# Kernel tuning notes

Measured on AMD Instinct MI355X. Metric: run time of the kernel, lower is better.

The kernel has to match this reference:

```python
import jax, jax.numpy as jnp
import numpy as np

# SOM hyperparameters (from init_kwargs)
M_ROWS = 64
N_COLS = 64
DIM = 256
MAX_EPOCHS = 100
INITIAL_RADIUS = 32.0  # max(m, n) / 2
INITIAL_LR = 0.1
STD_COEFF = 0.5
BATCH = 8192

# [m*n, 2] integer grid locations (constant, non-differentiable)
_LOC_VECTS = jnp.asarray(
    np.stack(np.meshgrid(np.arange(M_ROWS), np.arange(N_COLS), indexing='ij'), axis=-1).reshape(-1, 2),
    dtype=jnp.int32,
)


def setup_inputs() -> dict:
    key = jax.random.key(0)
    k1, k2 = jax.random.split(key)
    return {
        'input_vect': jax.random.normal(k1, (BATCH, DIM), dtype=jnp.float32),
        'weights': jax.random.normal(k2, (M_ROWS * N_COLS, DIM), dtype=jnp.float32),
        'epoch': 10,
    }


def reference(input_vect, weights, epoch):
    # squared_distance[b, m] = sum_d (weights[m, d] - x[b, d])^2  -> [B, M]
    sq_dist = (
        jnp.sum(input_vect * input_vect, axis=1, keepdims=True)
        - 2.0 * (input_vect @ weights.T)
        + jnp.sum(weights * weights, axis=1)[None, :]
    )
    bmu_indices = jnp.argmin(sq_dist, axis=1)             # [B]
    bmu_locs = _LOC_VECTS[bmu_indices]                    # [B, 2]

    ep = jnp.float32(epoch)
    radius = INITIAL_RADIUS - ep * ((INITIAL_RADIUS - 1.0) / (MAX_EPOCHS - 1.0))
    alpha = INITIAL_LR * (1.0 - ep / MAX_EPOCHS)

    # bmu_distance_squares[b, m] = ||locs[m] - bmu_locs[b]||^2  -> [B, M]
    diff = _LOC_VECTS[None, :, :] - bmu_locs[:, None, :]  # int [B, M, 2]
    bmu_dist_sq = jnp.sum(diff * diff, axis=2).astype(jnp.float32)

    denom_nf = 2.0 * jnp.square(radius * STD_COEFF)
    learning_rate_op = jnp.exp(-bmu_dist_sq / denom_nf) * alpha  # [B, M]

    # numerator[m, d] = sum_b lr[b, m] * x[b, d]
    numerator = jnp.einsum('bm,bd->md', learning_rate_op, input_vect)
    denominator = jnp.sum(learning_rate_op, axis=0)[:, None] + 1e-12  # [M, 1]
    new_weights = numerator / denominator
    return bmu_locs, new_weights
```

## Files before the change

kernel.cpp:

```cpp
#include <hip/hip_runtime.h>
#include <stdint.h>

#define DIM   256
#define BATCH 8192
#define MCELL 4096

typedef unsigned long long u64;
typedef unsigned short u16;
typedef __attribute__((ext_vector_type(8))) short bf16x8;
typedef __attribute__((ext_vector_type(4))) float f32x4;

__device__ __forceinline__ u64 packMin(float v, unsigned idx) {
    unsigned u = __float_as_uint(v);
    u = (u & 0x80000000u) ? ~u : (u | 0x80000000u);
    return ((u64)u << 32) | (u64)idx;
}
__device__ __forceinline__ u16 f2bf(float f) {
    unsigned u = __float_as_uint(f);
    u += 0x7fffu + ((u >> 16) & 1u);
    return (u16)(u >> 16);
}
__device__ __forceinline__ void gll16(const void* g, const char* l) {
    __builtin_amdgcn_global_load_lds(
        (const __attribute__((address_space(1))) unsigned int*)g,
        (__attribute__((address_space(3))) unsigned int*)l, 16, 0, 0);
}
__device__ __forceinline__ u64 umin64(u64 a, u64 b) { return a < b ? a : b; }
__device__ __forceinline__ u64 umax64(u64 a, u64 b) { return a < b ? b : a; }
__device__ __forceinline__ void merge3(u64& a1, u64& a2, u64& a3,
                                       u64 o1, u64 o2, u64 o3) {
    u64 L1 = umin64(a1, o1), H1 = umax64(a1, o1);
    u64 L2 = umin64(a2, o2);
    u64 L3 = umin64(a3, o3);
    a1 = L1;
    a2 = umin64(H1, L2);
    a3 = umin64(umax64(H1, L2), L3);
}

__global__ void k_prep(const float* __restrict__ X, const float* __restrict__ W,
                       u16* __restrict__ Xh, u16* __restrict__ Wh,
                       float* __restrict__ w2, const int* __restrict__ epoch_p,
                       float* __restrict__ scal) {
    const int blk = blockIdx.x;
    const int t = threadIdx.x;
    if (blk == 3072) {
        int raw = epoch_p[0];
        float ep = (raw >= 0 && raw < 100000) ? (float)raw : __int_as_float(raw);
        float radius = 32.0f - ep * (31.0f / 99.0f);
        float alpha  = 0.1f * (1.0f - ep / 100.0f);
        float rs = radius * 0.5f;
        float denom = 2.0f * rs * rs;
        if (t < 64)       scal[t]  = expf(-((float)(t * t)) / denom);
        else if (t == 64) scal[64] = alpha;
        return;
    }
    if (blk < 2048) {
        const int fi = blk * 256 + t;
        float4 v = ((const float4*)X)[fi];
        ushort4 h = {f2bf(v.x), f2bf(v.y), f2bf(v.z), f2bf(v.w)};
        ((ushort4*)Xh)[fi] = h;
    } else {
        const int fi = (blk - 2048) * 256 + t;
        float4 v = ((const float4*)W)[fi];
        ushort4 h = {f2bf(v.x), f2bf(v.y), f2bf(v.z), f2bf(v.w)};
        ((ushort4*)Wh)[fi] = h;
        float s = v.x * v.x + v.y * v.y + v.z * v.z + v.w * v.w;
        #pragma unroll
        for (int off = 32; off; off >>= 1) s += __shfl_down(s, off);
        if ((t & 63) == 0) w2[fi >> 6] = s;
    }
}

__global__ __launch_bounds__(256, 3)
void k_gemm_argmin(const u16* __restrict__ Xh, const u16* __restrict__ Wh,
                   const float* __restrict__ w2, u64* __restrict__ slots) {
    __shared__ char smem[49152];
    const int wg = blockIdx.x;
    const int swz = (wg & 7) * 256 + (wg >> 3);
    const int bt = swz >> 5;
    const int mt = swz & 31;
    const int tid = threadIdx.x;
    const int wid = tid >> 6;
    const int lane = tid & 63;
    const int wr = wid >> 1, wc = wid & 1;
    const int b0 = bt * 128, m0 = mt * 128;
    const int m0w = m0 + wc * 64;

    const int sr0 = wid * 32 + (lane >> 2);
    const int sr1 = sr0 + 16;
    const int ss  = lane & 3;
    const int sg0 = ss ^ ((sr0 >> 1) & 3);
    const int sg1 = ss ^ ((sr1 >> 1) & 3);
    const size_t gA0 = (size_t)(b0 + sr0) * DIM + sg0 * 8;
    const size_t gA1 = (size_t)(b0 + sr1) * DIM + sg1 * 8;
    const size_t gB0 = (size_t)(m0 + sr0) * DIM + sg0 * 8;
    const size_t gB1 = (size_t)(m0 + sr1) * DIM + sg1 * 8;
    const int ldsA = wid * 2048;

    const int rl = lane & 15, g = lane >> 4;
    const int slot = g ^ ((rl >> 1) & 3);
    const int aoff = (wr * 64 + rl) * 64 + slot * 16;
    const int boff = (wc * 64 + rl) * 64 + slot * 16;

    f32x4 acc[4][4];
    #pragma unroll
    for (int i = 0; i < 4; ++i)
        #pragma unroll
        for (int j = 0; j < 4; ++j) acc[i][j] = (f32x4){0.f, 0.f, 0.f, 0.f};

    #define STAGE(buf, c) do {                                                \
        char* base_ = smem + (buf) * 16384;                                   \
        const int co_ = (c) * 32;                                             \
        gll16(Xh + gA0 + co_, base_ + ldsA);                                  \
        gll16(Xh + gA1 + co_, base_ + ldsA + 1024);                           \
        gll16(Wh + gB0 + co_, base_ + 8192 + ldsA);                           \
        gll16(Wh + gB1 + co_, base_ + 8192 + ldsA + 1024);                    \
    } while (0)

    STAGE(0, 0);
    STAGE(1, 1);
    #pragma unroll
    for (int c = 0; c < 8; ++c) {
        if (c < 6) {
            STAGE((c + 2) % 3, c + 2);
            asm volatile("s_waitcnt vmcnt(8)" ::: "memory");
        } else if (c == 6) {
            asm volatile("s_waitcnt vmcnt(4)" ::: "memory");
        } else {
            asm volatile("s_waitcnt vmcnt(0)" ::: "memory");
        }
        __builtin_amdgcn_sched_barrier(0);
        __builtin_amdgcn_s_barrier();

        const char* bufc = smem + (c % 3) * 16384;
        bf16x8 ah[4];
        #pragma unroll
        for (int i = 0; i < 4; ++i)
            ah[i] = *(const bf16x8*)(bufc + aoff + i * 1024);
        __builtin_amdgcn_s_setprio(1);
        #pragma unroll
        for (int j = 0; j < 4; ++j) {
            const bf16x8 bh = *(const bf16x8*)(bufc + 8192 + boff + j * 1024);
            #pragma unroll
            for (int i = 0; i < 4; ++i)
                acc[i][j] = __builtin_amdgcn_mfma_f32_16x16x32_bf16(ah[i], bh, acc[i][j], 0, 0, 0);
        }
        __builtin_amdgcn_s_setprio(0);
        __builtin_amdgcn_s_barrier();
    }
    #undef STAGE

    float w2v[4];
    #pragma unroll
    for (int j = 0; j < 4; ++j) w2v[j] = w2[m0w + j * 16 + rl];

    __syncthreads();
    u64* ex = (u64*)smem;

    #pragma unroll
    for (int i = 0; i < 4; ++i) {
        #pragma unroll
        for (int q = 0; q < 4; ++q) {
            u64 t1 = ~0ull, t2 = ~0ull, t3 = ~0ull;
            #pragma unroll
            for (int j = 0; j < 4; ++j) {
                const float d = w2v[j] - 2.0f * acc[i][j][q];
                const u64 p = packMin(d, (unsigned)(m0w + j * 16 + rl));
                if (p < t1)      { t3 = t2; t2 = t1; t1 = p; }
                else if (p < t2) { t3 = t2; t2 = p; }
                else if (p < t3) { t3 = p; }
            }
            #pragma unroll
            for (int off = 1; off <= 8; off <<= 1) {
                const u64 o1 = __shfl_xor(t1, off);
                const u64 o2 = __shfl_xor(t2, off);
                const u64 o3 = __shfl_xor(t3, off);
                merge3(t1, t2, t3, o1, o2, o3);
            }
            if (rl == 0) {
                const int rloc = wr * 64 + i * 16 + g * 4 + q;
                u64* e = ex + (rloc * 2 + wc) * 3;
                e[0] = t1; e[1] = t2; e[2] = t3;
            }
        }
    }
    __syncthreads();
    if (tid < 128) {
        const u64* e0 = ex + (tid * 2 + 0) * 3;
        const u64* e1 = ex + (tid * 2 + 1) * 3;
        u64 a1 = e0[0], a2 = e0[1], a3 = e0[2];
        merge3(a1, a2, a3, e1[0], e1[1], e1[2]);
        const size_t row = b0 + tid;
        slots[row * 96 +      mt] = a1;
        slots[row * 96 + 32 + mt] = a2;
        slots[row * 96 + 64 + mt] = a3;
    }
}

__global__ void k_merge(const u64* __restrict__ slots, const float* __restrict__ X,
                        const float* __restrict__ W, const float* __restrict__ w2,
                        float* __restrict__ out_locs, float* __restrict__ A,
                        float* __restrict__ cnt) {
    const int wid = threadIdx.x >> 6, l = threadIdx.x & 63;
    const int row = blockIdx.x * 4 + wid;
    u64 t1, t2, t3;
    if (l < 32) {
        const u64* s = slots + (size_t)row * 96;
        t1 = s[l]; t2 = s[32 + l]; t3 = s[64 + l];
    } else { t1 = t2 = t3 = ~0ull; }
    #pragma unroll
    for (int off = 1; off <= 32; off <<= 1) {
        const u64 o1 = __shfl_xor(t1, off);
        const u64 o2 = __shfl_xor(t2, off);
        const u64 o3 = __shfl_xor(t3, off);
        merge3(t1, t2, t3, o1, o2, o3);
    }
    const int cand[3] = {(int)(t1 & 0xFFFFFFFFull), (int)(t2 & 0xFFFFFFFFull),
                         (int)(t3 & 0xFFFFFFFFull)};
    const float4 xv = *(const float4*)(X + (size_t)row * DIM + l * 4);
    float bd = 0.0f; int bm = -1;
    #pragma unroll
    for (int tix = 0; tix < 3; ++tix) {
        const int mc = cand[tix];
        const float4 wv = *(const float4*)(W + (size_t)mc * DIM + l * 4);
        float s = xv.x * wv.x + xv.y * wv.y + xv.z * wv.z + xv.w * wv.w;
        #pragma unroll
        for (int off = 1; off <= 32; off <<= 1) s += __shfl_xor(s, off);
        const float d = w2[mc] - 2.0f * s;
        if (bm < 0 || d < bd || (d == bd && mc < bm)) { bd = d; bm = mc; }
    }
    if (l == 0) {
        out_locs[row * 2 + 0] = (float)(bm >> 6);
        out_locs[row * 2 + 1] = (float)(bm & 63);
        atomicAdd(&cnt[bm], 1.0f);
    }
    float* ap = A + (size_t)bm * DIM + l * 4;
    atomicAdd(ap + 0, xv.x);
    atomicAdd(ap + 1, xv.y);
    atomicAdd(ap + 2, xv.z);
    atomicAdd(ap + 3, xv.w);
}

__global__ void k_conv1(const float* __restrict__ A, const float* __restrict__ E,
                        float* __restrict__ T1, const float* __restrict__ cnt,
                        float* __restrict__ c1) {
    if (blockIdx.x >= 4096) {
        int t = (blockIdx.x - 4096) * 256 + threadIdx.x;
        int gi = t >> 6, mj = t & 63;
        float acc = 0.0f;
        #pragma unroll
        for (int gj = 0; gj < 64; ++gj) {
            int dd = mj - gj; dd = dd < 0 ? -dd : dd;
            acc += E[dd] * cnt[gi * 64 + gj];
        }
        c1[gi * 64 + mj] = acc;
        return;
    }
    __shared__ float Es[64];
    const int d = threadIdx.x;
    if (d < 64) Es[d] = E[d];
    __syncthreads();
    const int gi = blockIdx.x >> 6, mj = blockIdx.x & 63;
    const float* base = A + (size_t)gi * 64 * DIM + d;
    float acc = 0.0f;
    #pragma unroll
    for (int gj = 0; gj < 64; ++gj) {
        int dd = mj - gj; dd = dd < 0 ? -dd : dd;
        acc += Es[dd] * base[(size_t)gj * DIM];
    }
    T1[(size_t)blockIdx.x * DIM + d] = acc;
}

__global__ void k_conv2(const float* __restrict__ T1, const float* __restrict__ scal,
                        const float* __restrict__ c1, float* __restrict__ outw) {
    __shared__ float Es[64];
    __shared__ float salpha;
    const int d = threadIdx.x;
    if (d < 64) Es[d] = scal[d];
    if (d == 64) salpha = scal[64];
    __syncthreads();
    const int mi = blockIdx.x >> 6, mj = blockIdx.x & 63;
    float acc = 0.0f, den = 0.0f;
    #pragma unroll
    for (int gi = 0; gi < 64; ++gi) {
        int dd = mi - gi; dd = dd < 0 ? -dd : dd;
        acc += Es[dd] * T1[((size_t)gi * 64 + mj) * DIM + d];
        den += Es[dd] * c1[gi * 64 + mj];
    }
    const float a = salpha;
    const float v = (a * acc) / (a * den + 1e-12f);
    outw[((size_t)mi * 64 + mj) * DIM + d] = v;
}

extern "C" void kernel_launch(void* const* d_in, const int* in_sizes, int n_in,
                              void* d_out, int out_size, void* d_ws, size_t ws_size,
                              hipStream_t stream) {
    const float* X = (const float*)d_in[0];
    const float* W = (const float*)d_in[1];
    const int*   ep = (const int*)d_in[2];
    float* out = (float*)d_out;

    char* ws = (char*)d_ws;
    u64*   slots = (u64*)(ws + 0);
    u16*   Xh   = (u16*)(ws + 6291456);
    float* A    = (float*)(ws + 6291456);
    float* cnt  = (float*)(ws + 10485760);
    u16*   Wh   = (u16*)(ws + 10502144);
    float* w2   = (float*)(ws + 12599296);
    float* scal = (float*)(ws + 12615680);
    float* c1   = (float*)(ws + 12616192);
    float* T1   = (float*)(ws + 0);

    k_prep<<<3073, 256, 0, stream>>>(X, W, Xh, Wh, w2, ep, scal);
    k_gemm_argmin<<<2048, 256, 0, stream>>>(Xh, Wh, w2, slots);
    hipMemsetAsync(ws + 6291456, 0, 4194304 + 16384, stream);
    k_merge<<<2048, 256, 0, stream>>>(slots, X, W, w2, out, A, cnt);
    k_conv1<<<4112, 256, 0, stream>>>(A, scal, T1, cnt, c1);
    k_conv2<<<4096, 256, 0, stream>>>(T1, scal, c1, out + 16384);
}
```

Measured before the change: 200.5 us.

## Transpose GEMM operand roles and keep top-2 candidates per tile instead of top-3

Swaps the MFMA operand roles so each lane's accumulators run along the codebook dimension for a fixed batch column. This lets each thread do most of the per-row argmin in registers and cuts the cross-lane shuffle reduction to two steps. Each tile now keeps the two best candidates instead of three, which shrinks the slots buffer and the merge kernel's loads. The merge kernel still refines the final candidates in exact fp32, but keeping fewer bf16 candidates raises the chance of picking a different BMU on near-ties.

```diff
diff --git a/kernel.cpp b/kernel.cpp
--- a/kernel.cpp
+++ b/kernel.cpp
@@ -27,6 +27,16 @@
 }
 __device__ __forceinline__ u64 umin64(u64 a, u64 b) { return a < b ? a : b; }
 __device__ __forceinline__ u64 umax64(u64 a, u64 b) { return a < b ? b : a; }
+__device__ __forceinline__ void ins2(u64& t1, u64& t2, u64 p) {
+    u64 hi = umax64(p, t1);
+    t1 = umin64(p, t1);
+    t2 = umin64(t2, hi);
+}
+__device__ __forceinline__ void merge2(u64& a1, u64& a2, u64 o1, u64 o2) {
+    u64 H1 = umax64(a1, o1);
+    a1 = umin64(a1, o1);
+    a2 = umin64(H1, umin64(a2, o2));
+}
 __device__ __forceinline__ void merge3(u64& a1, u64& a2, u64& a3,
                                        u64 o1, u64 o2, u64 o3) {
     u64 L1 = umin64(a1, o1), H1 = umax64(a1, o1);
@@ -84,7 +94,6 @@
     const int lane = tid & 63;
     const int wr = wid >> 1, wc = wid & 1;
     const int b0 = bt * 128, m0 = mt * 128;
-    const int m0w = m0 + wc * 64;
 
     const int sr0 = wid * 32 + (lane >> 2);
     const int sr1 = sr0 + 16;
@@ -99,8 +108,8 @@
 
     const int rl = lane & 15, g = lane >> 4;
     const int slot = g ^ ((rl >> 1) & 3);
-    const int aoff = (wr * 64 + rl) * 64 + slot * 16;
-    const int boff = (wc * 64 + rl) * 64 + slot * 16;
+    const int xoff = (wc * 64 + rl) * 64 + slot * 16;
+    const int woff = (wr * 64 + rl) * 64 + slot * 16;
 
     f32x4 acc[4][4];
     #pragma unroll
@@ -133,67 +142,59 @@
         __builtin_amdgcn_s_barrier();
 
         const char* bufc = smem + (c % 3) * 16384;
-        bf16x8 ah[4];
+        bf16x8 wf[4];
         #pragma unroll
         for (int i = 0; i < 4; ++i)
-            ah[i] = *(const bf16x8*)(bufc + aoff + i * 1024);
+            wf[i] = *(const bf16x8*)(bufc + 8192 + woff + i * 1024);
         __builtin_amdgcn_s_setprio(1);
         #pragma unroll
         for (int j = 0; j < 4; ++j) {
-            const bf16x8 bh = *(const bf16x8*)(bufc + 8192 + boff + j * 1024);
+            const bf16x8 xf = *(const bf16x8*)(bufc + xoff + j * 1024);
             #pragma unroll
             for (int i = 0; i < 4; ++i)
-                acc[i][j] = __builtin_amdgcn_mfma_f32_16x16x32_bf16(ah[i], bh, acc[i][j], 0, 0, 0);
+                acc[i][j] = __builtin_amdgcn_mfma_f32_16x16x32_bf16(wf[i], xf, acc[i][j], 0, 0, 0);
         }
         __builtin_amdgcn_s_setprio(0);
         __builtin_amdgcn_s_barrier();
     }
     #undef STAGE
 
-    float w2v[4];
-    #pragma unroll
-    for (int j = 0; j < 4; ++j) w2v[j] = w2[m0w + j * 16 + rl];
+    float w2v[16];
+    #pragma unroll
+    for (int ii = 0; ii < 16; ++ii)
+        w2v[ii] = w2[m0 + wr * 64 + (ii >> 2) * 16 + g * 4 + (ii & 3)];
 
     __syncthreads();
     u64* ex = (u64*)smem;
 
     #pragma unroll
-    for (int i = 0; i < 4; ++i) {
-        #pragma unroll
-        for (int q = 0; q < 4; ++q) {
-            u64 t1 = ~0ull, t2 = ~0ull, t3 = ~0ull;
+    for (int j = 0; j < 4; ++j) {
+        u64 t1 = ~0ull, t2 = ~0ull;
+        #pragma unroll
+        for (int i = 0; i < 4; ++i)
             #pragma unroll
-            for (int j = 0; j < 4; ++j) {
-                const float d = w2v[j] - 2.0f * acc[i][j][q];
-                const u64 p = packMin(d, (unsigned)(m0w + j * 16 + rl));
-                if (p < t1)      { t3 = t2; t2 = t1; t1 = p; }
-                else if (p < t2) { t3 = t2; t2 = p; }
-                else if (p < t3) { t3 = p; }
+            for (int q = 0; q < 4; ++q) {
+                const float d = fmaf(-2.0f, acc[i][j][q], w2v[i * 4 + q]);
+                ins2(t1, t2, packMin(d, (unsigned)(m0 + wr * 64 + i * 16 + g * 4 + q)));
             }
-            #pragma unroll
-            for (int off = 1; off <= 8; off <<= 1) {
-                const u64 o1 = __shfl_xor(t1, off);
-                const u64 o2 = __shfl_xor(t2, off);
-                const u64 o3 = __shfl_xor(t3, off);
-                merge3(t1, t2, t3, o1, o2, o3);
-            }
-            if (rl == 0) {
-                const int rloc = wr * 64 + i * 16 + g * 4 + q;
-                u64* e = ex + (rloc * 2 + wc) * 3;
-                e[0] = t1; e[1] = t2; e[2] = t3;
-            }
+        #pragma unroll
+        for (int off = 16; off <= 32; off <<= 1) {
+            const u64 o1 = __shfl_xor(t1, off);
+            const u64 o2 = __shfl_xor(t2, off);
+            merge2(t1, t2, o1, o2);
+        }
+        if (lane < 16) {
+            u64* e = ex + ((size_t)(wc * 64 + j * 16 + rl) * 2 + wr) * 2;
+            e[0] = t1; e[1] = t2;
         }
     }
     __syncthreads();
     if (tid < 128) {
-        const u64* e0 = ex + (tid * 2 + 0) * 3;
-        const u64* e1 = ex + (tid * 2 + 1) * 3;
-        u64 a1 = e0[0], a2 = e0[1], a3 = e0[2];
-        merge3(a1, a2, a3, e1[0], e1[1], e1[2]);
-        const size_t row = b0 + tid;
-        slots[row * 96 +      mt] = a1;
-        slots[row * 96 + 32 + mt] = a2;
-        slots[row * 96 + 64 + mt] = a3;
+        const u64* e = ex + (size_t)tid * 4;
+        u64 a1 = e[0], a2 = e[1];
+        merge2(a1, a2, e[2], e[3]);
+        slots[(size_t)(b0 + tid) * 64 + mt]      = a1;
+        slots[(size_t)(b0 + tid) * 64 + 32 + mt] = a2;
     }
 }
 
@@ -203,11 +204,7 @@
                         float* __restrict__ cnt) {
     const int wid = threadIdx.x >> 6, l = threadIdx.x & 63;
     const int row = blockIdx.x * 4 + wid;
-    u64 t1, t2, t3;
-    if (l < 32) {
-        const u64* s = slots + (size_t)row * 96;
-        t1 = s[l]; t2 = s[32 + l]; t3 = s[64 + l];
-    } else { t1 = t2 = t3 = ~0ull; }
+    u64 t1 = slots[(size_t)row * 64 + l], t2 = ~0ull, t3 = ~0ull;
     #pragma unroll
     for (int off = 1; off <= 32; off <<= 1) {
         const u64 o1 = __shfl_xor(t1, off);
@@ -302,18 +299,18 @@
 
     char* ws = (char*)d_ws;
     u64*   slots = (u64*)(ws + 0);
-    u16*   Xh   = (u16*)(ws + 6291456);
-    float* A    = (float*)(ws + 6291456);
-    float* cnt  = (float*)(ws + 10485760);
-    u16*   Wh   = (u16*)(ws + 10502144);
-    float* w2   = (float*)(ws + 12599296);
-    float* scal = (float*)(ws + 12615680);
-    float* c1   = (float*)(ws + 12616192);
-    float* T1   = (float*)(ws + 0);
+    float* T1    = (float*)(ws + 0);
+    u16*   Xh    = (u16*)(ws + (4u << 20));
+    float* A     = (float*)(ws + (4u << 20));
+    float* cnt   = (float*)(ws + (8u << 20));
+    u16*   Wh    = (u16*)(ws + (8u << 20) + 16384);
+    float* w2    = (float*)(ws + (10u << 20) + 16384);
+    float* scal  = (float*)(ws + (10u << 20) + 32768);
+    float* c1    = (float*)(ws + (10u << 20) + 36864);
 
     k_prep<<<3073, 256, 0, stream>>>(X, W, Xh, Wh, w2, ep, scal);
     k_gemm_argmin<<<2048, 256, 0, stream>>>(Xh, Wh, w2, slots);
-    hipMemsetAsync(ws + 6291456, 0, 4194304 + 16384, stream);
+    hipMemsetAsync(ws + (4u << 20), 0, (4u << 20) + 16384, stream);
     k_merge<<<2048, 256, 0, stream>>>(slots, X, W, w2, out, A, cnt);
     k_conv1<<<4112, 256, 0, stream>>>(A, scal, T1, cnt, c1);
     k_conv2<<<4096, 256, 0, stream>>>(T1, scal, c1, out + 16384);
```

Measured after the change: 172.8 us. 13.8% less time.
